# Optimization experiments

Measured on AMD Instinct MI355X. Metric: run time of the kernel, lower is better.

## Reference

```python
import math
import jax, jax.numpy as jnp
import numpy as np

B, L, D = 8, 512, 32
SEQ_LEN = 512.0
N_PATCHES, N_REF = 16, 32
LAT, HM = 128, 4
FH, NL, FF = 8, 3, 128
PRED = 96

def _time_embed(t, d):
    # interleaved sin/cos embedding, matching PositionalEmbedding's div_term
    div = jnp.exp(jnp.arange(0, d, 2, dtype=jnp.float32) * (-math.log(10000.0) / d))
    ang = t[..., None] * div
    out = jnp.zeros(t.shape + (d,), dtype=jnp.float32)
    return out.at[..., 0::2].set(jnp.sin(ang)).at[..., 1::2].set(jnp.cos(ang))

def _layernorm(x, g, b):
    mu = jnp.mean(x, axis=-1, keepdims=True)
    var = jnp.var(x, axis=-1, keepdims=True)
    return (x - mu) / jnp.sqrt(var + 1e-5) * g + b

def _mha(z, Wq, Wk, Wv, Wo, bq, bk, bv, bo):
    N, S, dm = z.shape
    hd = dm // FH
    q = (z @ Wq + bq).reshape(N, S, FH, hd)
    k = (z @ Wk + bk).reshape(N, S, FH, hd)
    v = (z @ Wv + bv).reshape(N, S, FH, hd)
    s = jnp.einsum('nqhe,nkhe->nhqk', q, k) / math.sqrt(hd)
    a = jax.nn.softmax(s, axis=-1)
    o = jnp.einsum('nhqk,nkhe->nqhe', a, v).reshape(N, S, dm)
    return o @ Wo + bo

def _forward(x, x_mark, x_mask, Wq, Wk, W_out, b_out, f_Wq, f_Wk, f_Wv, f_Wo, f_bq, f_bk, f_bv, f_bo, f_ln1_g, f_ln1_b, f_W1, f_b1, f_W2, f_b2, f_ln2_g, f_ln2_b, ln_f_g, ln_f_b, W_lin, b_lin):
    t = x_mark[:, :, 0]                                   # [B, L] irregular timestamps in [0, SEQ_LEN]
    edges = jnp.linspace(0.0, SEQ_LEN, N_PATCHES + 1)
    refs = jnp.linspace(0.0, SEQ_LEN, N_REF * N_PATCHES).reshape(N_PATCHES, N_REF)
    obs_valid = jnp.sum(x_mask, axis=-1) > 0              # [B, L]
    dk = LAT // HM
    Kmat = (_time_embed(t, LAT) @ Wk).reshape(B, L, HM, dk)
    v = x * x_mask                                        # mask values like `v = v * m` in original
    reprs = []
    for i in range(N_PATCHES):  # fixed small structural loop
        # _split_patch equivalent: per-channel masked attention is permutation
        # invariant, so the sort/scatter compaction reduces to masking.
        in_patch = (t >= edges[i]) & (t <= edges[i + 1]) & obs_valid   # [B, L]
        Qi = (_time_embed(refs[i], LAT) @ Wq).reshape(N_REF, HM, dk)
        scores = jnp.einsum('rhe,blhe->bhrl', Qi, Kmat) / math.sqrt(dk)
        cmask = x_mask * in_patch[..., None].astype(x.dtype)           # [B, L, D]
        neg = jnp.where(cmask[:, None, None, :, :] > 0, 0.0, -1e9)     # [B,1,1,L,D]
        p = jax.nn.softmax(scores[..., None] + neg, axis=3)            # [B,H,R,L,D]
        attn = jnp.einsum('bhrld,bld->brhd', p, v)                     # [B,R,H,D]
        reprs.append(attn.reshape(B, N_REF, HM * D) @ W_out + b_out)   # [B,R,D]
    rp = jnp.stack(reprs, axis=1)                          # [B, NP, R, D]
    z = rp.transpose(0, 3, 1, 2).reshape(B * D, N_PATCHES, N_REF)
    z = z + _time_embed(jnp.arange(N_PATCHES, dtype=jnp.float32), N_REF)[None]
    for l in range(NL):
        a = _mha(z, f_Wq[l], f_Wk[l], f_Wv[l], f_Wo[l], f_bq[l], f_bk[l], f_bv[l], f_bo[l])
        z = _layernorm(z + a, f_ln1_g[l], f_ln1_b[l])
        y = jax.nn.gelu(z @ f_W1[l] + f_b1[l]) @ f_W2[l] + f_b2[l]
        z = _layernorm(z + y, f_ln2_g[l], f_ln2_b[l])
    z = _layernorm(z, ln_f_g, ln_f_b)
    emb = z.reshape(B, D, N_PATCHES, N_REF).transpose(0, 1, 3, 2)      # [B, D, R, NP]
    out = emb.reshape(B, D, N_REF * N_PATCHES) @ W_lin + b_lin         # [B, D, PRED]
    return out.transpose(0, 2, 1)                          # [B, PRED, D]

def setup_inputs():
    key = jax.random.key(0)
    ks = jax.random.split(key, 30)
    def w(i, shape, fan_in):
        return jax.random.normal(ks[i], shape, jnp.float32) / math.sqrt(fan_in)
    return {
        'x': jax.random.normal(ks[0], (B, L, D), jnp.float32),
        'x_mark': jnp.sort(jax.random.uniform(ks[1], (B, L, 1), jnp.float32) * SEQ_LEN, axis=1),
        'x_mask': (jax.random.uniform(ks[2], (B, L, D), jnp.float32) < 0.8).astype(jnp.float32),
        'Wq': w(3, (LAT, LAT), LAT),
        'Wk': w(4, (LAT, LAT), LAT),
        'W_out': w(5, (HM * D, D), HM * D),
        'b_out': jnp.zeros((D,), jnp.float32),
        'f_Wq': w(6, (NL, N_REF, N_REF), N_REF),
        'f_Wk': w(7, (NL, N_REF, N_REF), N_REF),
        'f_Wv': w(8, (NL, N_REF, N_REF), N_REF),
        'f_Wo': w(9, (NL, N_REF, N_REF), N_REF),
        'f_bq': jnp.zeros((NL, N_REF), jnp.float32),
        'f_bk': jnp.zeros((NL, N_REF), jnp.float32),
        'f_bv': jnp.zeros((NL, N_REF), jnp.float32),
        'f_bo': jnp.zeros((NL, N_REF), jnp.float32),
        'f_ln1_g': jnp.ones((NL, N_REF), jnp.float32),
        'f_ln1_b': jnp.zeros((NL, N_REF), jnp.float32),
        'f_W1': w(10, (NL, N_REF, FF), N_REF),
        'f_b1': jnp.zeros((NL, FF), jnp.float32),
        'f_W2': w(11, (NL, FF, N_REF), FF),
        'f_b2': jnp.zeros((NL, N_REF), jnp.float32),
        'f_ln2_g': jnp.ones((NL, N_REF), jnp.float32),
        'f_ln2_b': jnp.zeros((NL, N_REF), jnp.float32),
        'ln_f_g': jnp.ones((N_REF,), jnp.float32),
        'ln_f_b': jnp.zeros((N_REF,), jnp.float32),
        'W_lin': w(12, (N_REF * N_PATCHES, PRED), N_REF * N_PATCHES),
        'b_lin': jnp.zeros((PRED,), jnp.float32),
    }

def reference(x, x_mark, x_mask, Wq, Wk, W_out, b_out, f_Wq, f_Wk, f_Wv, f_Wo, f_bq, f_bk, f_bv, f_bo, f_ln1_g, f_ln1_b, f_W1, f_b1, f_W2, f_b2, f_ln2_g, f_ln2_b, ln_f_g, ln_f_b, W_lin, b_lin):
    return _forward(x, x_mark, x_mask, Wq, Wk, W_out, b_out, f_Wq, f_Wk, f_Wv, f_Wo, f_bq, f_bk, f_bv, f_bo, f_ln1_g, f_ln1_b, f_W1, f_b1, f_W2, f_b2, f_ln2_g, f_ln2_b, ln_f_g, ln_f_b, W_lin, b_lin)
```

## Files before the change

### kernel.cpp

```cpp
#include <hip/hip_runtime.h>
#include <math.h>


#define ISQ32 0.17677669529663687f
#define C128  (-0.07195578415606394f)
#define C32   (-0.28782313662425575f)

__global__ void k_embed_mm(const float* __restrict__ x_mark,
                           const float* __restrict__ Wk,
                           const float* __restrict__ Wq,
                           const float* __restrict__ x_mask,
                           float* __restrict__ Kmat,
                           float* __restrict__ Qall,
                           unsigned* __restrict__ obsBits) {
    __shared__ float sTe[4][128];
    if (blockIdx.x >= 1152) {
        const int gt = (blockIdx.x - 1152) * 256 + threadIdx.x;
        const int w = gt >> 6, lane = gt & 63;
        const int bl = w * 2 + (lane >> 5);
        const int d = lane & 31;
        const unsigned long long mm = __ballot(x_mask[bl * 32 + d] > 0.0f);
        if (lane == 0)  obsBits[w * 2]     = (unsigned)(mm & 0xffffffffull);
        if (lane == 32) obsBits[w * 2 + 1] = (unsigned)(mm >> 32);
        return;
    }
    const int wave = threadIdx.x >> 6;
    const int lane = threadIdx.x & 63;
    const int row = blockIdx.x * 4 + wave;
    float t;
    const float* W;
    float* outp;
    if (row < 4096) {
        t = x_mark[row];
        W = Wk;
        outp = Kmat + row * 128;
    } else {
        const int qr = row - 4096;
        t = (float)qr * (512.0f / 511.0f);
        W = Wq;
        outp = Qall + qr * 128;
    }
    const float dv = expf((float)(2 * lane) * C128);
    const float ang = t * dv;
    sTe[wave][2 * lane]     = sinf(ang);
    sTe[wave][2 * lane + 1] = cosf(ang);
    __syncthreads();
    float a0 = 0.f, a1 = 0.f;
    #pragma unroll 8
    for (int k = 0; k < 128; ++k) {
        const float te = sTe[wave][k];
        a0 = fmaf(te, W[k * 128 + lane], a0);
        a1 = fmaf(te, W[k * 128 + lane + 64], a1);
    }
    outp[lane] = a0;
    outp[lane + 64] = a1;
}

__launch_bounds__(256)
__global__ void k_patch_attn(const float* __restrict__ x,
                             const float* __restrict__ x_mark,
                             const unsigned* __restrict__ obsBits,
                             const float* __restrict__ Kmat,
                             const float* __restrict__ Qall,
                             float* __restrict__ attn) {
    __shared__ float sQ[32][36];
    __shared__ float sK[96][36];
    __shared__ float sX[96][36];
    __shared__ float sS[32][100];
    __shared__ unsigned sBits[96];
    __shared__ int sLo, sHi;
    __shared__ unsigned sAV;
    const int tid = threadIdx.x;
    const int h = blockIdx.x & 3;
    const int b = (blockIdx.x >> 2) & 7;
    const int i = blockIdx.x >> 5;
    const float e0 = 32.0f * (float)i, e1 = 32.0f * (float)(i + 1);
    if (tid == 0) { sLo = 512; sHi = -1; sAV = 0u; }
    __syncthreads();
    #pragma unroll
    for (int k = 0; k < 4; ++k) {
        const int idx = tid + 256 * k;
        sQ[idx >> 5][idx & 31] = Qall[(i * 32 + (idx >> 5)) * 128 + h * 32 + (idx & 31)];
    }
    {
        int mylo = 512, myhi = -1;
        unsigned mybits = 0u;
        #pragma unroll
        for (int k = 0; k < 2; ++k) {
            const int l = tid + 256 * k;
            const float t = x_mark[b * 512 + l];
            if (t >= e0 && t <= e1) {
                mylo = min(mylo, l);
                myhi = max(myhi, l);
                mybits |= obsBits[b * 512 + l];
            }
        }
        #pragma unroll
        for (int off = 32; off > 0; off >>= 1) {
            mylo = min(mylo, __shfl_xor(mylo, off));
            myhi = max(myhi, __shfl_xor(myhi, off));
            mybits |= __shfl_xor(mybits, off);
        }
        if ((tid & 63) == 0) {
            atomicMin(&sLo, mylo);
            atomicMax(&sHi, myhi);
            atomicOr(&sAV, mybits);
        }
    }
    __syncthreads();
    const int lo = sLo, hi = sHi;
    const int NA = hi - lo + 1;
    const unsigned av = sAV;
    const int r = tid >> 3, dg = tid & 7;

    if (NA >= 1 && NA <= 96 && av == 0xffffffffu) {
        if (tid < NA) sBits[tid] = obsBits[b * 512 + lo + tid];
        for (int idx = tid; idx < NA * 32; idx += 256) {
            const int ll = idx >> 5, c = idx & 31;
            sK[ll][c] = Kmat[(b * 512 + lo + ll) * 128 + h * 32 + c];
            sX[ll][c] = x[(b * 512 + lo + ll) * 32 + c];
        }
        __syncthreads();
        float m = -1e30f;
        for (int ll = dg; ll < NA; ll += 8) {
            float p0 = 0.f, p1 = 0.f, p2 = 0.f, p3 = 0.f;
            #pragma unroll
            for (int e = 0; e < 32; e += 4) {
                p0 = fmaf(sQ[r][e],     sK[ll][e],     p0);
                p1 = fmaf(sQ[r][e + 1], sK[ll][e + 1], p1);
                p2 = fmaf(sQ[r][e + 2], sK[ll][e + 2], p2);
                p3 = fmaf(sQ[r][e + 3], sK[ll][e + 3], p3);
            }
            const float s = (p0 + p1 + p2 + p3) * ISQ32;
            sS[r][ll] = s;
            m = fmaxf(m, s);
        }
        #pragma unroll
        for (int off = 4; off > 0; off >>= 1) m = fmaxf(m, __shfl_xor(m, off));
        for (int ll = dg; ll < NA; ll += 8) sS[r][ll] = __expf(sS[r][ll] - m);
        __syncthreads();
        float num0 = 0.f, num1 = 0.f, num2 = 0.f, num3 = 0.f;
        float den0 = 0.f, den1 = 0.f, den2 = 0.f, den3 = 0.f;
        for (int ll = 0; ll < NA; ++ll) {
            const float e = sS[r][ll];
            const unsigned bits = sBits[ll];
            if ((bits >> dg) & 1u)        { den0 += e; num0 = fmaf(e, sX[ll][dg],      num0); }
            if ((bits >> (dg + 8)) & 1u)  { den1 += e; num1 = fmaf(e, sX[ll][dg + 8],  num1); }
            if ((bits >> (dg + 16)) & 1u) { den2 += e; num2 = fmaf(e, sX[ll][dg + 16], num2); }
            if ((bits >> (dg + 24)) & 1u) { den3 += e; num3 = fmaf(e, sX[ll][dg + 24], num3); }
        }
        float* ap = attn + ((i * 8 + b) * 32 + r) * 128 + h * 32;
        ap[dg]      = num0 / den0;
        ap[dg + 8]  = num1 / den1;
        ap[dg + 16] = num2 / den2;
        ap[dg + 24] = num3 / den3;
    } else {
        float m = -1e30f;
        float num[4] = {0.f, 0.f, 0.f, 0.f}, den[4] = {0.f, 0.f, 0.f, 0.f};
        for (int l = 0; l < 512; ++l) {
            const float t = x_mark[b * 512 + l];
            const unsigned bits = obsBits[b * 512 + l];
            const bool inr = (t >= e0 && t <= e1);
            const unsigned effD = (inr ? bits : 0u) | ~av;
            if (effD == 0u) continue;
            const unsigned effN = effD & bits;
            const float* Kp = Kmat + (b * 512 + l) * 128 + h * 32;
            float a = 0.f;
            #pragma unroll
            for (int e2 = 0; e2 < 32; ++e2) a = fmaf(sQ[r][e2], Kp[e2], a);
            const float s = a * ISQ32;
            float eNew;
            if (s > m) {
                const float scale = __expf(m - s);
                #pragma unroll
                for (int j = 0; j < 4; ++j) { den[j] *= scale; num[j] *= scale; }
                m = s;
                eNew = 1.0f;
            } else {
                eNew = __expf(s - m);
            }
            const float* xp = x + (b * 512 + l) * 32;
            #pragma unroll
            for (int j = 0; j < 4; ++j) {
                const int d = dg + 8 * j;
                if ((effD >> d) & 1u) den[j] += eNew;
                if ((effN >> d) & 1u) num[j] = fmaf(eNew, xp[d], num[j]);
            }
        }
        float* ap = attn + ((i * 8 + b) * 32 + r) * 128 + h * 32;
        #pragma unroll
        for (int j = 0; j < 4; ++j) ap[dg + 8 * j] = num[j] / den[j];
    }
}

__global__ void k_reprs(const float* __restrict__ attn,
                        const float* __restrict__ W_out,
                        const float* __restrict__ b_out,
                        float* __restrict__ z) {
    __shared__ float sA[32][129];
    const int tid = threadIdx.x;
    const int b = blockIdx.x & 7;
    const int i = blockIdx.x >> 3;
    #pragma unroll
    for (int k = 0; k < 16; ++k) {
        const int idx = tid + 256 * k;
        sA[idx >> 7][idx & 127] = attn[(i * 8 + b) * 4096 + idx];
    }
    __syncthreads();
    const int r = tid & 31, dgrp = tid >> 5;
    float acc0 = 0.f, acc1 = 0.f, acc2 = 0.f, acc3 = 0.f;
    #pragma unroll 8
    for (int k = 0; k < 128; ++k) {
        const float a = sA[r][k];
        acc0 = fmaf(a, W_out[k * 32 + dgrp],      acc0);
        acc1 = fmaf(a, W_out[k * 32 + dgrp + 8],  acc1);
        acc2 = fmaf(a, W_out[k * 32 + dgrp + 16], acc2);
        acc3 = fmaf(a, W_out[k * 32 + dgrp + 24], acc3);
    }
    const float dv = expf((float)(2 * (r >> 1)) * C32);
    const float ang = (float)i * dv;
    const float pe = (r & 1) ? cosf(ang) : sinf(ang);
    const int base = i * 32 + r;
    z[(b * 32 + dgrp)      * 512 + base] = acc0 + b_out[dgrp]      + pe;
    z[(b * 32 + dgrp + 8)  * 512 + base] = acc1 + b_out[dgrp + 8]  + pe;
    z[(b * 32 + dgrp + 16) * 512 + base] = acc2 + b_out[dgrp + 16] + pe;
    z[(b * 32 + dgrp + 24) * 512 + base] = acc3 + b_out[dgrp + 24] + pe;
}

__launch_bounds__(256, 1)
__global__ void k_former(const float* __restrict__ z,
                         const float* __restrict__ f_Wq, const float* __restrict__ f_Wk,
                         const float* __restrict__ f_Wv, const float* __restrict__ f_Wo,
                         const float* __restrict__ f_bq, const float* __restrict__ f_bk,
                         const float* __restrict__ f_bv, const float* __restrict__ f_bo,
                         const float* __restrict__ f_ln1_g, const float* __restrict__ f_ln1_b,
                         const float* __restrict__ f_W1, const float* __restrict__ f_b1,
                         const float* __restrict__ f_W2, const float* __restrict__ f_b2,
                         const float* __restrict__ f_ln2_g, const float* __restrict__ f_ln2_b,
                         const float* __restrict__ ln_f_g, const float* __restrict__ ln_f_b,
                         const float* __restrict__ W_lin, const float* __restrict__ b_lin,
                         float* __restrict__ out) {
    __shared__ float sZ[16][32];
    __shared__ float sQ[16][33], sK[16][33], sV[16][33];
    __shared__ float sO[16][32];
    __shared__ float sH[16][128];
    __shared__ float sZf[512];
    __shared__ float sPart[2][96];
    const int tid = threadIdx.x;
    const int n = blockIdx.x;
    const int j = tid & 31, s2 = tid >> 5;
    const int sA = s2 * 2, sB = sA + 1;

    #pragma unroll
    for (int k = 0; k < 2; ++k) {
        const int idx = tid + 256 * k;
        sZ[idx >> 5][idx & 31] = z[n * 512 + idx];
    }
    float zlocA = z[n * 512 + sA * 32 + j];
    float zlocB = z[n * 512 + sB * 32 + j];
    __syncthreads();

    for (int layer = 0; layer < 3; ++layer) {
        const float* Wq = f_Wq + layer * 1024;
        const float* Wk = f_Wk + layer * 1024;
        const float* Wv = f_Wv + layer * 1024;
        const float* Wo = f_Wo + layer * 1024;
        const float* W1 = f_W1 + layer * 4096;
        const float* W2 = f_W2 + layer * 4096;

        {
            float wq[32], wk[32], wv[32];
            #pragma unroll
            for (int k = 0; k < 32; ++k) {
                wq[k] = Wq[k * 32 + j];
                wk[k] = Wk[k * 32 + j];
                wv[k] = Wv[k * 32 + j];
            }
            float qa = f_bq[layer * 32 + j], qb = qa;
            float ka = f_bk[layer * 32 + j], kb = ka;
            float va = f_bv[layer * 32 + j], vb = va;
            const float4* zra = (const float4*)&sZ[sA][0];
            const float4* zrb = (const float4*)&sZ[sB][0];
            #pragma unroll
            for (int k4 = 0; k4 < 8; ++k4) {
                const float4 a = zra[k4], b4 = zrb[k4];
                qa = fmaf(a.x, wq[4*k4], qa);   qa = fmaf(a.y, wq[4*k4+1], qa);
                qa = fmaf(a.z, wq[4*k4+2], qa); qa = fmaf(a.w, wq[4*k4+3], qa);
                qb = fmaf(b4.x, wq[4*k4], qb);   qb = fmaf(b4.y, wq[4*k4+1], qb);
                qb = fmaf(b4.z, wq[4*k4+2], qb); qb = fmaf(b4.w, wq[4*k4+3], qb);
                ka = fmaf(a.x, wk[4*k4], ka);   ka = fmaf(a.y, wk[4*k4+1], ka);
                ka = fmaf(a.z, wk[4*k4+2], ka); ka = fmaf(a.w, wk[4*k4+3], ka);
                kb = fmaf(b4.x, wk[4*k4], kb);   kb = fmaf(b4.y, wk[4*k4+1], kb);
                kb = fmaf(b4.z, wk[4*k4+2], kb); kb = fmaf(b4.w, wk[4*k4+3], kb);
                va = fmaf(a.x, wv[4*k4], va);   va = fmaf(a.y, wv[4*k4+1], va);
                va = fmaf(a.z, wv[4*k4+2], va); va = fmaf(a.w, wv[4*k4+3], va);
                vb = fmaf(b4.x, wv[4*k4], vb);   vb = fmaf(b4.y, wv[4*k4+1], vb);
                vb = fmaf(b4.z, wv[4*k4+2], vb); vb = fmaf(b4.w, wv[4*k4+3], vb);
            }
            sQ[sA][j] = qa; sQ[sB][j] = qb;
            sK[sA][j] = ka; sK[sB][j] = kb;
            sV[sA][j] = va; sV[sB][j] = vb;
        }
        __syncthreads();
        if (tid < 128) {
            const int hh = tid >> 4, q = tid & 15;
            float sc[16];
            float mx = -1e30f;
            #pragma unroll
            for (int k = 0; k < 16; ++k) {
                float a = 0.f;
                #pragma unroll
                for (int e = 0; e < 4; ++e) a = fmaf(sQ[q][hh * 4 + e], sK[k][hh * 4 + e], a);
                sc[k] = a * 0.5f;
                mx = fmaxf(mx, sc[k]);
            }
            float sum = 0.f;
            #pragma unroll
            for (int k = 0; k < 16; ++k) { sc[k] = __expf(sc[k] - mx); sum += sc[k]; }
            const float inv = 1.0f / sum;
            #pragma unroll
            for (int e = 0; e < 4; ++e) {
                float a = 0.f;
                #pragma unroll
                for (int k = 0; k < 16; ++k) a = fmaf(sc[k], sV[k][hh * 4 + e], a);
                sO[q][hh * 4 + e] = a * inv;
            }
        }
        __syncthreads();
        {
            float wo[32];
            #pragma unroll
            for (int k = 0; k < 32; ++k) wo[k] = Wo[k * 32 + j];
            float oa = f_bo[layer * 32 + j], ob = oa;
            const float4* ora = (const float4*)&sO[sA][0];
            const float4* orb = (const float4*)&sO[sB][0];
            #pragma unroll
            for (int k4 = 0; k4 < 8; ++k4) {
                const float4 a = ora[k4], b4 = orb[k4];
                oa = fmaf(a.x, wo[4*k4], oa);   oa = fmaf(a.y, wo[4*k4+1], oa);
                oa = fmaf(a.z, wo[4*k4+2], oa); oa = fmaf(a.w, wo[4*k4+3], oa);
                ob = fmaf(b4.x, wo[4*k4], ob);   ob = fmaf(b4.y, wo[4*k4+1], ob);
                ob = fmaf(b4.z, wo[4*k4+2], ob); ob = fmaf(b4.w, wo[4*k4+3], ob);
            }
            const float tA = zlocA + oa, tB = zlocB + ob;
            float sumA = tA, sqA = tA * tA, sumB = tB, sqB = tB * tB;
            #pragma unroll
            for (int off = 16; off > 0; off >>= 1) {
                sumA += __shfl_xor(sumA, off); sqA += __shfl_xor(sqA, off);
                sumB += __shfl_xor(sumB, off); sqB += __shfl_xor(sqB, off);
            }
            const float muA = sumA * (1.0f / 32.0f);
            const float rsA = rsqrtf(sqA * (1.0f / 32.0f) - muA * muA + 1e-5f);
            const float muB = sumB * (1.0f / 32.0f);
            const float rsB = rsqrtf(sqB * (1.0f / 32.0f) - muB * muB + 1e-5f);
            const float g1 = f_ln1_g[layer * 32 + j], be1 = f_ln1_b[layer * 32 + j];
            zlocA = (tA - muA) * rsA * g1 + be1;
            zlocB = (tB - muB) * rsB * g1 + be1;
            sZ[sA][j] = zlocA;
            sZ[sB][j] = zlocB;
        }
        __syncthreads();
        {
            const int f = tid & 127, sh = tid >> 7;
            float w1c[32];
            #pragma unroll
            for (int k = 0; k < 32; ++k) w1c[k] = W1[k * 128 + f];
            const float b1v = f_b1[layer * 128 + f];
            #pragma unroll
            for (int ss = 0; ss < 8; ++ss) {
                const int s = sh * 8 + ss;
                const float4* zr = (const float4*)&sZ[s][0];
                float acc = b1v;
                #pragma unroll
                for (int k4 = 0; k4 < 8; ++k4) {
                    const float4 a = zr[k4];
                    acc = fmaf(a.x, w1c[4*k4], acc);   acc = fmaf(a.y, w1c[4*k4+1], acc);
                    acc = fmaf(a.z, w1c[4*k4+2], acc); acc = fmaf(a.w, w1c[4*k4+3], acc);
                }
                const float c = acc;
                const float a2 = 1.5957691216057308f * (c + 0.044715f * c * c * c);
                const float e = __expf(a2);
                const float th = 1.0f - 2.0f / (e + 1.0f);
                sH[s][f] = 0.5f * c * (1.0f + th);
            }
        }
        float w2c[128];
        #pragma unroll
        for (int k = 0; k < 128; ++k) w2c[k] = W2[k * 32 + j];
        __syncthreads();
        {
            float fa = f_b2[layer * 32 + j], fb = fa;
            const float4* hra = (const float4*)&sH[sA][0];
            const float4* hrb = (const float4*)&sH[sB][0];
            #pragma unroll
            for (int k4 = 0; k4 < 32; ++k4) {
                const float4 a = hra[k4], b4 = hrb[k4];
                fa = fmaf(a.x, w2c[4*k4], fa);   fa = fmaf(a.y, w2c[4*k4+1], fa);
                fa = fmaf(a.z, w2c[4*k4+2], fa); fa = fmaf(a.w, w2c[4*k4+3], fa);
                fb = fmaf(b4.x, w2c[4*k4], fb);   fb = fmaf(b4.y, w2c[4*k4+1], fb);
                fb = fmaf(b4.z, w2c[4*k4+2], fb); fb = fmaf(b4.w, w2c[4*k4+3], fb);
            }
            const float tA = zlocA + fa, tB = zlocB + fb;
            float sumA = tA, sqA = tA * tA, sumB = tB, sqB = tB * tB;
            #pragma unroll
            for (int off = 16; off > 0; off >>= 1) {
                sumA += __shfl_xor(sumA, off); sqA += __shfl_xor(sqA, off);
                sumB += __shfl_xor(sumB, off); sqB += __shfl_xor(sqB, off);
            }
            const float muA = sumA * (1.0f / 32.0f);
            const float rsA = rsqrtf(sqA * (1.0f / 32.0f) - muA * muA + 1e-5f);
            const float muB = sumB * (1.0f / 32.0f);
            const float rsB = rsqrtf(sqB * (1.0f / 32.0f) - muB * muB + 1e-5f);
            const float g2 = f_ln2_g[layer * 32 + j], be2 = f_ln2_b[layer * 32 + j];
            zlocA = (tA - muA) * rsA * g2 + be2;
            zlocB = (tB - muB) * rsB * g2 + be2;
            sZ[sA][j] = zlocA;
            sZ[sB][j] = zlocB;
        }
        __syncthreads();
    }
    {
        float sumA = zlocA, sqA = zlocA * zlocA, sumB = zlocB, sqB = zlocB * zlocB;
        #pragma unroll
        for (int off = 16; off > 0; off >>= 1) {
            sumA += __shfl_xor(sumA, off); sqA += __shfl_xor(sqA, off);
            sumB += __shfl_xor(sumB, off); sqB += __shfl_xor(sqB, off);
        }
        const float muA = sumA * (1.0f / 32.0f);
        const float rsA = rsqrtf(sqA * (1.0f / 32.0f) - muA * muA + 1e-5f);
        const float muB = sumB * (1.0f / 32.0f);
        const float rsB = rsqrtf(sqB * (1.0f / 32.0f) - muB * muB + 1e-5f);
        const float gf = ln_f_g[j], bf = ln_f_b[j];
        sZf[j * 16 + sA] = (zlocA - muA) * rsA * gf + bf;
        sZf[j * 16 + sB] = (zlocB - muB) * rsB * gf + bf;
    }
    __syncthreads();
    if (tid < 192) {
        const int half = tid / 96, o = tid % 96;
        const int j0 = half * 256;
        float acc = 0.f;
        #pragma unroll 8
        for (int jj = 0; jj < 256; ++jj)
            acc = fmaf(sZf[j0 + jj], W_lin[(j0 + jj) * 96 + o], acc);
        sPart[half][o] = acc;
    }
    __syncthreads();
    if (tid < 96)
        out[((n >> 5) * 96 + tid) * 32 + (n & 31)] = sPart[0][tid] + sPart[1][tid] + b_lin[tid];
}

extern "C" void kernel_launch(void* const* d_in, const int* in_sizes, int n_in,
                              void* d_out, int out_size, void* d_ws, size_t ws_size,
                              hipStream_t stream) {
    const float* x       = (const float*)d_in[0];
    const float* x_mark  = (const float*)d_in[1];
    const float* x_mask  = (const float*)d_in[2];
    const float* Wq      = (const float*)d_in[3];
    const float* Wk      = (const float*)d_in[4];
    const float* W_out   = (const float*)d_in[5];
    const float* b_out   = (const float*)d_in[6];
    const float* f_Wq    = (const float*)d_in[7];
    const float* f_Wk    = (const float*)d_in[8];
    const float* f_Wv    = (const float*)d_in[9];
    const float* f_Wo    = (const float*)d_in[10];
    const float* f_bq    = (const float*)d_in[11];
    const float* f_bk    = (const float*)d_in[12];
    const float* f_bv    = (const float*)d_in[13];
    const float* f_bo    = (const float*)d_in[14];
    const float* f_ln1_g = (const float*)d_in[15];
    const float* f_ln1_b = (const float*)d_in[16];
    const float* f_W1    = (const float*)d_in[17];
    const float* f_b1    = (const float*)d_in[18];
    const float* f_W2    = (const float*)d_in[19];
    const float* f_b2    = (const float*)d_in[20];
    const float* f_ln2_g = (const float*)d_in[21];
    const float* f_ln2_b = (const float*)d_in[22];
    const float* ln_f_g  = (const float*)d_in[23];
    const float* ln_f_b  = (const float*)d_in[24];
    const float* W_lin   = (const float*)d_in[25];
    const float* b_lin   = (const float*)d_in[26];

    float* ws = (float*)d_ws;
    float* Kmat      = ws;
    float* Qall      = ws + 524288;
    unsigned* obsB   = (unsigned*)(ws + 589824);
    float* attn      = ws + 593920;
    float* zbuf      = ws + 1118208;

    k_embed_mm<<<1664, 256, 0, stream>>>(x_mark, Wk, Wq, x_mask, Kmat, Qall, obsB);
    k_patch_attn<<<512, 256, 0, stream>>>(x, x_mark, obsB, Kmat, Qall, attn);
    k_reprs<<<128, 256, 0, stream>>>(attn, W_out, b_out, zbuf);
    k_former<<<256, 256, 0, stream>>>(zbuf,
        f_Wq, f_Wk, f_Wv, f_Wo, f_bq, f_bk, f_bv, f_bo,
        f_ln1_g, f_ln1_b, f_W1, f_b1, f_W2, f_b2, f_ln2_g, f_ln2_b,
        ln_f_g, ln_f_b, W_lin, b_lin, (float*)d_out);
}
```

Before: 70.36 us.

## Register-block embed matmul rows and stage former weights in shared memory with prefetch

The embedding matmul now has each wave compute 8 rows, so every weight load feeds 8 FMAs, and it uses fast sin/cos/exp intrinsics. The block count drops accordingly. The transformer kernel stages each layer's QKV/O/FFN weights in shared memory cooperatively with float4 loads, replacing per-thread strided global loads, and prefetches the next layer's weights into registers during compute. Attention output work is spread over all 256 threads. The fast intrinsics may slightly change numerics, and the extra shared memory and registers could lower occupancy.

After: 72.83 us. 1.04x slower.

```diff
diff --git a/kernel.cpp b/kernel.cpp
--- a/kernel.cpp
+++ b/kernel.cpp
@@ -6,6 +6,7 @@
 #define C128  (-0.07195578415606394f)
 #define C32   (-0.28782313662425575f)
 
+__launch_bounds__(256)
 __global__ void k_embed_mm(const float* __restrict__ x_mark,
                            const float* __restrict__ Wk,
                            const float* __restrict__ Wq,
@@ -13,9 +14,8 @@
                            float* __restrict__ Kmat,
                            float* __restrict__ Qall,
                            unsigned* __restrict__ obsBits) {
-    __shared__ float sTe[4][128];
-    if (blockIdx.x >= 1152) {
-        const int gt = (blockIdx.x - 1152) * 256 + threadIdx.x;
+    if (blockIdx.x >= 144) {
+        const int gt = (blockIdx.x - 144) * 256 + threadIdx.x;
         const int w = gt >> 6, lane = gt & 63;
         const int bl = w * 2 + (lane >> 5);
         const int d = lane & 31;
@@ -24,36 +24,42 @@
         if (lane == 32) obsBits[w * 2 + 1] = (unsigned)(mm >> 32);
         return;
     }
-    const int wave = threadIdx.x >> 6;
+    __shared__ float sTe[32][128];
+    const int wv = threadIdx.x >> 6;
     const int lane = threadIdx.x & 63;
-    const int row = blockIdx.x * 4 + wave;
-    float t;
-    const float* W;
-    float* outp;
-    if (row < 4096) {
-        t = x_mark[row];
-        W = Wk;
-        outp = Kmat + row * 128;
-    } else {
-        const int qr = row - 4096;
-        t = (float)qr * (512.0f / 511.0f);
-        W = Wq;
-        outp = Qall + qr * 128;
-    }
-    const float dv = expf((float)(2 * lane) * C128);
-    const float ang = t * dv;
-    sTe[wave][2 * lane]     = sinf(ang);
-    sTe[wave][2 * lane + 1] = cosf(ang);
-    __syncthreads();
-    float a0 = 0.f, a1 = 0.f;
-    #pragma unroll 8
+    const int bb = blockIdx.x;
+    const int row0 = bb * 32 + wv * 8;
+    const float dv = __expf((float)(2 * lane) * C128);
+    #pragma unroll
+    for (int rr = 0; rr < 8; ++rr) {
+        const int row = row0 + rr;
+        const float t = (row < 4096) ? x_mark[row] : (float)(row - 4096) * (512.0f / 511.0f);
+        const float ang = t * dv;
+        sTe[wv * 8 + rr][2 * lane]     = __sinf(ang);
+        sTe[wv * 8 + rr][2 * lane + 1] = __cosf(ang);
+    }
+    __syncthreads();
+    const float* W = (bb < 128) ? Wk : Wq;
+    float a0[8], a1[8];
+    #pragma unroll
+    for (int rr = 0; rr < 8; ++rr) { a0[rr] = 0.f; a1[rr] = 0.f; }
     for (int k = 0; k < 128; ++k) {
-        const float te = sTe[wave][k];
-        a0 = fmaf(te, W[k * 128 + lane], a0);
-        a1 = fmaf(te, W[k * 128 + lane + 64], a1);
-    }
-    outp[lane] = a0;
-    outp[lane + 64] = a1;
+        const float wa = W[k * 128 + lane];
+        const float wb = W[k * 128 + lane + 64];
+        #pragma unroll
+        for (int rr = 0; rr < 8; ++rr) {
+            const float te = sTe[wv * 8 + rr][k];
+            a0[rr] = fmaf(te, wa, a0[rr]);
+            a1[rr] = fmaf(te, wb, a1[rr]);
+        }
+    }
+    #pragma unroll
+    for (int rr = 0; rr < 8; ++rr) {
+        const int row = row0 + rr;
+        float* outp = (row < 4096) ? (Kmat + row * 128) : (Qall + (row - 4096) * 128);
+        outp[lane] = a0[rr];
+        outp[lane + 64] = a1[rr];
+    }
 }
 
 __launch_bounds__(256)
@@ -173,7 +179,7 @@
             if (s > m) {
                 const float scale = __expf(m - s);
                 #pragma unroll
-                for (int j = 0; j < 4; ++j) { den[j] *= scale; num[j] *= scale; }
+                for (int jj = 0; jj < 4; ++jj) { den[jj] *= scale; num[jj] *= scale; }
                 m = s;
                 eNew = 1.0f;
             } else {
@@ -181,15 +187,15 @@
             }
             const float* xp = x + (b * 512 + l) * 32;
             #pragma unroll
-            for (int j = 0; j < 4; ++j) {
-                const int d = dg + 8 * j;
-                if ((effD >> d) & 1u) den[j] += eNew;
-                if ((effN >> d) & 1u) num[j] = fmaf(eNew, xp[d], num[j]);
+            for (int jj = 0; jj < 4; ++jj) {
+                const int d = dg + 8 * jj;
+                if ((effD >> d) & 1u) den[jj] += eNew;
+                if ((effN >> d) & 1u) num[jj] = fmaf(eNew, xp[d], num[jj]);
             }
         }
         float* ap = attn + ((i * 8 + b) * 32 + r) * 128 + h * 32;
         #pragma unroll
-        for (int j = 0; j < 4; ++j) ap[dg + 8 * j] = num[j] / den[j];
+        for (int jj = 0; jj < 4; ++jj) ap[dg + 8 * jj] = num[jj] / den[jj];
     }
 }
 
@@ -226,6 +232,20 @@
     z[(b * 32 + dgrp + 16) * 512 + base] = acc2 + b_out[dgrp + 16] + pe;
     z[(b * 32 + dgrp + 24) * 512 + base] = acc3 + b_out[dgrp + 24] + pe;
 }
+
+#define QKV6(ax, bx, kk) { \
+    const float wq_ = sWq[(kk) * 32 + j]; \
+    const float wk_ = sWk[(kk) * 32 + j]; \
+    const float wv_ = sWv[(kk) * 32 + j]; \
+    qa = fmaf(ax, wq_, qa); qb = fmaf(bx, wq_, qb); \
+    ka = fmaf(ax, wk_, ka); kb = fmaf(bx, wk_, kb); \
+    va = fmaf(ax, wv_, va); vb = fmaf(bx, wv_, vb); }
+#define OP2(ax, bx, kk) { \
+    const float w_ = sWo[(kk) * 32 + j]; \
+    oa = fmaf(ax, w_, oa); ob = fmaf(bx, w_, ob); }
+#define F2(ax, bx, kk) { \
+    const float w_ = sW2[(kk) * 32 + j]; \
+    fa = fmaf(ax, w_, fa); fb = fmaf(bx, w_, fb); }
 
 __launch_bounds__(256, 1)
 __global__ void k_former(const float* __restrict__ z,
@@ -240,8 +260,10 @@
                          const float* __restrict__ ln_f_g, const float* __restrict__ ln_f_b,
                          const float* __restrict__ W_lin, const float* __restrict__ b_lin,
                          float* __restrict__ out) {
+    __shared__ float sWq[1024], sWk[1024], sWv[1024], sWo[1024];
+    __shared__ float sW1[4096], sW2[4096];
     __shared__ float sZ[16][32];
-    __shared__ float sQ[16][33], sK[16][33], sV[16][33];
+    __shared__ float sQs[16][33], sKs[16][33], sVs[16][33];
     __shared__ float sO[16][32];
     __shared__ float sH[16][128];
     __shared__ float sZf[512];
@@ -250,6 +272,9 @@
     const int n = blockIdx.x;
     const int j = tid & 31, s2 = tid >> 5;
     const int sA = s2 * 2, sB = sA + 1;
+    const int g = tid >> 6, t64 = tid & 63;
+    const float* Wg = (g == 0) ? f_Wq : ((g == 1) ? f_Wk : ((g == 2) ? f_Wv : f_Wo));
+    float* dstg = (g == 0) ? sWq : ((g == 1) ? sWk : ((g == 2) ? sWv : sWo));
 
     #pragma unroll
     for (int k = 0; k < 2; ++k) {
@@ -258,59 +283,61 @@
     }
     float zlocA = z[n * 512 + sA * 32 + j];
     float zlocB = z[n * 512 + sB * 32 + j];
-    __syncthreads();
-
+    {
+        float4 rq[4], r1[4], r2[4];
+        #pragma unroll
+        for (int rep = 0; rep < 4; ++rep) rq[rep] = ((const float4*)Wg)[rep * 64 + t64];
+        #pragma unroll
+        for (int rep = 0; rep < 4; ++rep) r1[rep] = ((const float4*)f_W1)[rep * 256 + tid];
+        #pragma unroll
+        for (int rep = 0; rep < 4; ++rep) r2[rep] = ((const float4*)f_W2)[rep * 256 + tid];
+        #pragma unroll
+        for (int rep = 0; rep < 4; ++rep) ((float4*)dstg)[rep * 64 + t64] = rq[rep];
+        #pragma unroll
+        for (int rep = 0; rep < 4; ++rep) ((float4*)sW1)[rep * 256 + tid] = r1[rep];
+        #pragma unroll
+        for (int rep = 0; rep < 4; ++rep) ((float4*)sW2)[rep * 256 + tid] = r2[rep];
+    }
+    __syncthreads();
+
+    float4 nq[4], n1[4], n2[4];
     for (int layer = 0; layer < 3; ++layer) {
-        const float* Wq = f_Wq + layer * 1024;
-        const float* Wk = f_Wk + layer * 1024;
-        const float* Wv = f_Wv + layer * 1024;
-        const float* Wo = f_Wo + layer * 1024;
-        const float* W1 = f_W1 + layer * 4096;
-        const float* W2 = f_W2 + layer * 4096;
-
+        if (layer < 2) {
+            const int offQ = (layer + 1) * 1024, offF = (layer + 1) * 4096;
+            #pragma unroll
+            for (int rep = 0; rep < 4; ++rep) nq[rep] = ((const float4*)(Wg + offQ))[rep * 64 + t64];
+            #pragma unroll
+            for (int rep = 0; rep < 4; ++rep) n1[rep] = ((const float4*)(f_W1 + offF))[rep * 256 + tid];
+            #pragma unroll
+            for (int rep = 0; rep < 4; ++rep) n2[rep] = ((const float4*)(f_W2 + offF))[rep * 256 + tid];
+        }
         {
-            float wq[32], wk[32], wv[32];
-            #pragma unroll
-            for (int k = 0; k < 32; ++k) {
-                wq[k] = Wq[k * 32 + j];
-                wk[k] = Wk[k * 32 + j];
-                wv[k] = Wv[k * 32 + j];
-            }
-            float qa = f_bq[layer * 32 + j], qb = qa;
-            float ka = f_bk[layer * 32 + j], kb = ka;
-            float va = f_bv[layer * 32 + j], vb = va;
+            const float bq = f_bq[layer * 32 + j], bk = f_bk[layer * 32 + j], bv = f_bv[layer * 32 + j];
+            float qa = 0.f, qb = 0.f, ka = 0.f, kb = 0.f, va = 0.f, vb = 0.f;
             const float4* zra = (const float4*)&sZ[sA][0];
             const float4* zrb = (const float4*)&sZ[sB][0];
             #pragma unroll
             for (int k4 = 0; k4 < 8; ++k4) {
                 const float4 a = zra[k4], b4 = zrb[k4];
-                qa = fmaf(a.x, wq[4*k4], qa);   qa = fmaf(a.y, wq[4*k4+1], qa);
-                qa = fmaf(a.z, wq[4*k4+2], qa); qa = fmaf(a.w, wq[4*k4+3], qa);
-                qb = fmaf(b4.x, wq[4*k4], qb);   qb = fmaf(b4.y, wq[4*k4+1], qb);
-                qb = fmaf(b4.z, wq[4*k4+2], qb); qb = fmaf(b4.w, wq[4*k4+3], qb);
-                ka = fmaf(a.x, wk[4*k4], ka);   ka = fmaf(a.y, wk[4*k4+1], ka);
-                ka = fmaf(a.z, wk[4*k4+2], ka); ka = fmaf(a.w, wk[4*k4+3], ka);
-                kb = fmaf(b4.x, wk[4*k4], kb);   kb = fmaf(b4.y, wk[4*k4+1], kb);
-                kb = fmaf(b4.z, wk[4*k4+2], kb); kb = fmaf(b4.w, wk[4*k4+3], kb);
-                va = fmaf(a.x, wv[4*k4], va);   va = fmaf(a.y, wv[4*k4+1], va);
-                va = fmaf(a.z, wv[4*k4+2], va); va = fmaf(a.w, wv[4*k4+3], va);
-                vb = fmaf(b4.x, wv[4*k4], vb);   vb = fmaf(b4.y, wv[4*k4+1], vb);
-                vb = fmaf(b4.z, wv[4*k4+2], vb); vb = fmaf(b4.w, wv[4*k4+3], vb);
-            }
-            sQ[sA][j] = qa; sQ[sB][j] = qb;
-            sK[sA][j] = ka; sK[sB][j] = kb;
-            sV[sA][j] = va; sV[sB][j] = vb;
-        }
-        __syncthreads();
-        if (tid < 128) {
-            const int hh = tid >> 4, q = tid & 15;
+                QKV6(a.x, b4.x, 4 * k4 + 0)
+                QKV6(a.y, b4.y, 4 * k4 + 1)
+                QKV6(a.z, b4.z, 4 * k4 + 2)
+                QKV6(a.w, b4.w, 4 * k4 + 3)
+            }
+            sQs[sA][j] = qa + bq; sQs[sB][j] = qb + bq;
+            sKs[sA][j] = ka + bk; sKs[sB][j] = kb + bk;
+            sVs[sA][j] = va + bv; sVs[sB][j] = vb + bv;
+        }
+        __syncthreads();
+        {
+            const int q = tid & 15, hh = (tid >> 4) & 7, half = tid >> 7;
             float sc[16];
             float mx = -1e30f;
             #pragma unroll
             for (int k = 0; k < 16; ++k) {
                 float a = 0.f;
                 #pragma unroll
-                for (int e = 0; e < 4; ++e) a = fmaf(sQ[q][hh * 4 + e], sK[k][hh * 4 + e], a);
+                for (int e = 0; e < 4; ++e) a = fmaf(sQs[q][hh * 4 + e], sKs[k][hh * 4 + e], a);
                 sc[k] = a * 0.5f;
                 mx = fmaxf(mx, sc[k]);
             }
@@ -319,30 +346,30 @@
             for (int k = 0; k < 16; ++k) { sc[k] = __expf(sc[k] - mx); sum += sc[k]; }
             const float inv = 1.0f / sum;
             #pragma unroll
-            for (int e = 0; e < 4; ++e) {
+            for (int m = 0; m < 2; ++m) {
+                const int e = half * 2 + m;
                 float a = 0.f;
                 #pragma unroll
-                for (int k = 0; k < 16; ++k) a = fmaf(sc[k], sV[k][hh * 4 + e], a);
+                for (int k = 0; k < 16; ++k) a = fmaf(sc[k], sVs[k][hh * 4 + e], a);
                 sO[q][hh * 4 + e] = a * inv;
             }
         }
         __syncthreads();
         {
-            float wo[32];
-            #pragma unroll
-            for (int k = 0; k < 32; ++k) wo[k] = Wo[k * 32 + j];
-            float oa = f_bo[layer * 32 + j], ob = oa;
+            const float bo = f_bo[layer * 32 + j];
+            const float g1 = f_ln1_g[layer * 32 + j], be1 = f_ln1_b[layer * 32 + j];
+            float oa = 0.f, ob = 0.f;
             const float4* ora = (const float4*)&sO[sA][0];
             const float4* orb = (const float4*)&sO[sB][0];
             #pragma unroll
             for (int k4 = 0; k4 < 8; ++k4) {
                 const float4 a = ora[k4], b4 = orb[k4];
-                oa = fmaf(a.x, wo[4*k4], oa);   oa = fmaf(a.y, wo[4*k4+1], oa);
-                oa = fmaf(a.z, wo[4*k4+2], oa); oa = fmaf(a.w, wo[4*k4+3], oa);
-                ob = fmaf(b4.x, wo[4*k4], ob);   ob = fmaf(b4.y, wo[4*k4+1], ob);
-                ob = fmaf(b4.z, wo[4*k4+2], ob); ob = fmaf(b4.w, wo[4*k4+3], ob);
-            }
-            const float tA = zlocA + oa, tB = zlocB + ob;
+                OP2(a.x, b4.x, 4 * k4 + 0)
+                OP2(a.y, b4.y, 4 * k4 + 1)
+                OP2(a.z, b4.z, 4 * k4 + 2)
+                OP2(a.w, b4.w, 4 * k4 + 3)
+            }
+            const float tA = zlocA + oa + bo, tB = zlocB + ob + bo;
             float sumA = tA, sqA = tA * tA, sumB = tB, sqB = tB * tB;
             #pragma unroll
             for (int off = 16; off > 0; off >>= 1) {
@@ -353,7 +380,6 @@
             const float rsA = rsqrtf(sqA * (1.0f / 32.0f) - muA * muA + 1e-5f);
             const float muB = sumB * (1.0f / 32.0f);
             const float rsB = rsqrtf(sqB * (1.0f / 32.0f) - muB * muB + 1e-5f);
-            const float g1 = f_ln1_g[layer * 32 + j], be1 = f_ln1_b[layer * 32 + j];
             zlocA = (tA - muA) * rsA * g1 + be1;
             zlocB = (tB - muB) * rsB * g1 + be1;
             sZ[sA][j] = zlocA;
@@ -362,10 +388,10 @@
         __syncthreads();
         {
             const int f = tid & 127, sh = tid >> 7;
+            const float b1v = f_b1[layer * 128 + f];
             float w1c[32];
             #pragma unroll
-            for (int k = 0; k < 32; ++k) w1c[k] = W1[k * 128 + f];
-            const float b1v = f_b1[layer * 128 + f];
+            for (int k = 0; k < 32; ++k) w1c[k] = sW1[k * 128 + f];
             #pragma unroll
             for (int ss = 0; ss < 8; ++ss) {
                 const int s = sh * 8 + ss;
@@ -374,33 +400,31 @@
                 #pragma unroll
                 for (int k4 = 0; k4 < 8; ++k4) {
                     const float4 a = zr[k4];
-                    acc = fmaf(a.x, w1c[4*k4], acc);   acc = fmaf(a.y, w1c[4*k4+1], acc);
-                    acc = fmaf(a.z, w1c[4*k4+2], acc); acc = fmaf(a.w, w1c[4*k4+3], acc);
+                    acc = fmaf(a.x, w1c[4 * k4], acc);     acc = fmaf(a.y, w1c[4 * k4 + 1], acc);
+                    acc = fmaf(a.z, w1c[4 * k4 + 2], acc); acc = fmaf(a.w, w1c[4 * k4 + 3], acc);
                 }
                 const float c = acc;
                 const float a2 = 1.5957691216057308f * (c + 0.044715f * c * c * c);
                 const float e = __expf(a2);
-                const float th = 1.0f - 2.0f / (e + 1.0f);
-                sH[s][f] = 0.5f * c * (1.0f + th);
-            }
-        }
-        float w2c[128];
-        #pragma unroll
-        for (int k = 0; k < 128; ++k) w2c[k] = W2[k * 32 + j];
+                sH[s][f] = 0.5f * c * (2.0f - 2.0f / (e + 1.0f));
+            }
+        }
         __syncthreads();
         {
-            float fa = f_b2[layer * 32 + j], fb = fa;
+            const float b2v = f_b2[layer * 32 + j];
+            const float g2 = f_ln2_g[layer * 32 + j], be2 = f_ln2_b[layer * 32 + j];
+            float fa = 0.f, fb = 0.f;
             const float4* hra = (const float4*)&sH[sA][0];
             const float4* hrb = (const float4*)&sH[sB][0];
             #pragma unroll
             for (int k4 = 0; k4 < 32; ++k4) {
                 const float4 a = hra[k4], b4 = hrb[k4];
-                fa = fmaf(a.x, w2c[4*k4], fa);   fa = fmaf(a.y, w2c[4*k4+1], fa);
-                fa = fmaf(a.z, w2c[4*k4+2], fa); fa = fmaf(a.w, w2c[4*k4+3], fa);
-                fb = fmaf(b4.x, w2c[4*k4], fb);   fb = fmaf(b4.y, w2c[4*k4+1], fb);
-                fb = fmaf(b4.z, w2c[4*k4+2], fb); fb = fmaf(b4.w, w2c[4*k4+3], fb);
-            }
-            const float tA = zlocA + fa, tB = zlocB + fb;
+                F2(a.x, b4.x, 4 * k4 + 0)
+                F2(a.y, b4.y, 4 * k4 + 1)
+                F2(a.z, b4.z, 4 * k4 + 2)
+                F2(a.w, b4.w, 4 * k4 + 3)
+            }
+            const float tA = zlocA + fa + b2v, tB = zlocB + fb + b2v;
             float sumA = tA, sqA = tA * tA, sumB = tB, sqB = tB * tB;
             #pragma unroll
             for (int off = 16; off > 0; off >>= 1) {
@@ -411,13 +435,21 @@
             const float rsA = rsqrtf(sqA * (1.0f / 32.0f) - muA * muA + 1e-5f);
             const float muB = sumB * (1.0f / 32.0f);
             const float rsB = rsqrtf(sqB * (1.0f / 32.0f) - muB * muB + 1e-5f);
-            const float g2 = f_ln2_g[layer * 32 + j], be2 = f_ln2_b[layer * 32 + j];
             zlocA = (tA - muA) * rsA * g2 + be2;
             zlocB = (tB - muB) * rsB * g2 + be2;
             sZ[sA][j] = zlocA;
             sZ[sB][j] = zlocB;
         }
         __syncthreads();
+        if (layer < 2) {
+            #pragma unroll
+            for (int rep = 0; rep < 4; ++rep) ((float4*)dstg)[rep * 64 + t64] = nq[rep];
+            #pragma unroll
+            for (int rep = 0; rep < 4; ++rep) ((float4*)sW1)[rep * 256 + tid] = n1[rep];
+            #pragma unroll
+            for (int rep = 0; rep < 4; ++rep) ((float4*)sW2)[rep * 256 + tid] = n2[rep];
+            __syncthreads();
+        }
     }
     {
         float sumA = zlocA, sqA = zlocA * zlocA, sumB = zlocB, sqB = zlocB * zlocB;
@@ -439,7 +471,7 @@
         const int half = tid / 96, o = tid % 96;
         const int j0 = half * 256;
         float acc = 0.f;
-        #pragma unroll 8
+        #pragma unroll 16
         for (int jj = 0; jj < 256; ++jj)
             acc = fmaf(sZf[j0 + jj], W_lin[(j0 + jj) * 96 + o], acc);
         sPart[half][o] = acc;
@@ -487,7 +519,7 @@
     float* attn      = ws + 593920;
     float* zbuf      = ws + 1118208;
 
-    k_embed_mm<<<1664, 256, 0, stream>>>(x_mark, Wk, Wq, x_mask, Kmat, Qall, obsB);
+    k_embed_mm<<<656, 256, 0, stream>>>(x_mark, Wk, Wq, x_mask, Kmat, Qall, obsB);
     k_patch_attn<<<512, 256, 0, stream>>>(x, x_mark, obsB, Kmat, Qall, attn);
     k_reprs<<<128, 256, 0, stream>>>(attn, W_out, b_out, zbuf);
     k_former<<<256, 256, 0, stream>>>(zbuf,
```
